# Kernel tuning notes

Measured on AMD Instinct MI355X. Metric: run time of the kernel, lower is better.

The kernel has to match this reference:

```python
import jax, jax.numpy as jnp
import numpy as np

N_EMBED = 64
HEAD_SIZE = 64
B, T = 4096, 128

def setup_inputs() -> dict:
    key = jax.random.key(0)
    k0, k1, k2, k3 = jax.random.split(key, 4)
    x = jax.random.normal(k0, (B, T, N_EMBED), dtype=jnp.float32)
    # nn.Linear(N_EMBED, head_size, bias=False): weight shape [head_size, N_EMBED], y = x @ W.T
    Wq = jax.random.normal(k1, (HEAD_SIZE, N_EMBED), dtype=jnp.float32) * (1.0 / np.sqrt(N_EMBED))
    Wk = jax.random.normal(k2, (HEAD_SIZE, N_EMBED), dtype=jnp.float32) * (1.0 / np.sqrt(N_EMBED))
    Wv = jax.random.normal(k3, (HEAD_SIZE, N_EMBED), dtype=jnp.float32) * (1.0 / np.sqrt(N_EMBED))
    return {"x": x, "Wq": Wq, "Wk": Wk, "Wv": Wv}

def reference(x, Wq, Wk, Wv):
    # q,k,v: [B,T,H]
    q = jnp.einsum('btc,hc->bth', x, Wq)
    k = jnp.einsum('btc,hc->bth', x, Wk)
    v = jnp.einsum('btc,hc->bth', x, Wv)
    scale = HEAD_SIZE ** -0.5
    scores = jnp.einsum('bth,bsh->bts', q, k) * scale  # [B,T,T]
    Tdim = x.shape[1]
    causal = jnp.tril(jnp.ones((Tdim, Tdim), dtype=bool))
    scores = jnp.where(causal, scores, -jnp.inf)
    weights = jax.nn.softmax(scores, axis=-1)
    # dropout disabled (eval mode) for deterministic reference
    out = jnp.einsum('bts,bsh->bth', weights, v)  # [B,T,H]
    return out
```

## Files before the change

kernel.cpp:

```cpp
#include <hip/hip_runtime.h>

#define KS 76
#define VS 140

typedef float f4  __attribute__((ext_vector_type(4)));
typedef short s8v __attribute__((ext_vector_type(8)));
typedef short s4v __attribute__((ext_vector_type(4)));

#define MFMA16(a, b, c) __builtin_amdgcn_mfma_f32_16x16x32_bf16((a), (b), (c), 0, 0, 0)

__device__ __forceinline__ unsigned short f2bf(float f) {
  union { float f; unsigned u; } x; x.f = f;
  unsigned r = x.u + 0x7FFFu + ((x.u >> 16) & 1u);
  return (unsigned short)(r >> 16);
}
__device__ __forceinline__ float bf2f(unsigned short s) {
  union { unsigned u; float f; } x; x.u = ((unsigned)s) << 16; return x.f;
}
__device__ __forceinline__ s8v cvt8(const float* p) {
  float4 a = *(const float4*)p;
  float4 b = *(const float4*)(p + 4);
  s8v v;
  v[0] = (short)f2bf(a.x); v[1] = (short)f2bf(a.y);
  v[2] = (short)f2bf(a.z); v[3] = (short)f2bf(a.w);
  v[4] = (short)f2bf(b.x); v[5] = (short)f2bf(b.y);
  v[6] = (short)f2bf(b.z); v[7] = (short)f2bf(b.w);
  return v;
}
__device__ __forceinline__ unsigned pack2(float a, float b) {
  return (unsigned)f2bf(a) | ((unsigned)f2bf(b) << 16);
}
__device__ __forceinline__ s8v mk8(unsigned a0, unsigned a1, unsigned b0, unsigned b1) {
  union { unsigned u[4]; s8v v; } r;
  r.u[0] = a0; r.u[1] = a1; r.u[2] = b0; r.u[3] = b1;
  return r.v;
}
__device__ __forceinline__ s8v ld44(const short* p0, const short* p1) {
  s4v a = *(const s4v*)p0;
  s4v b = *(const s4v*)(p1);
  s8v r;
  r[0] = a[0]; r[1] = a[1]; r[2] = a[2]; r[3] = a[3];
  r[4] = b[0]; r[5] = b[1]; r[6] = b[2]; r[7] = b[3];
  return r;
}

__global__ __launch_bounds__(256, 3)
void attn_head(const void* __restrict__ xg, const void* __restrict__ wqg,
               const void* __restrict__ wkg, const void* __restrict__ wvg,
               void* __restrict__ outg) {
  __shared__ __align__(16) short smem[18688];
  short* Ksm = smem;
  short* Vt  = smem + 9728;

  const int tid  = threadIdx.x;
  const int wave = tid >> 6;
  const int lane = tid & 63;
  const int c16  = lane & 15;
  const int quad = lane >> 4;
  const int b    = blockIdx.x;

  int ok;
  {
    const unsigned short* w = (const unsigned short*)wqg;
    float f = bf2f(w[tid]);
    float a = fabsf(f);
    ok = (f == 0.0f || (a >= 1e-4f && a <= 1e4f)) ? 1 : 0;
  }
  const int isbf = (__syncthreads_count(ok) >= 230) ? 1 : 0;

  const int mts[2] = {wave, 7 - wave};

  s8v xf[2][2];
  #pragma unroll
  for (int mi = 0; mi < 2; mi++) {
    const size_t base = (size_t)b * (128 * 64) + (size_t)(mts[mi] * 16 + c16) * 64;
    #pragma unroll
    for (int kt = 0; kt < 2; kt++) {
      const int off = kt * 32 + quad * 8;
      if (isbf) xf[mi][kt] = *(const s8v*)((const unsigned short*)xg + base + off);
      else      xf[mi][kt] = cvt8((const float*)xg + base + off);
    }
  }

  f4 QT[2][4];
  #pragma unroll
  for (int ht = 0; ht < 4; ht++) {
    s8v wqf[2], wkf[2], wvf[2];
    const int woff0 = (ht * 16 + c16) * 64 + quad * 8;
    #pragma unroll
    for (int kt = 0; kt < 2; kt++) {
      const int off = woff0 + kt * 32;
      if (isbf) {
        wqf[kt] = *(const s8v*)((const unsigned short*)wqg + off);
        wkf[kt] = *(const s8v*)((const unsigned short*)wkg + off);
        wvf[kt] = *(const s8v*)((const unsigned short*)wvg + off);
      } else {
        wqf[kt] = cvt8((const float*)wqg + off);
        wkf[kt] = cvt8((const float*)wkg + off);
        wvf[kt] = cvt8((const float*)wvg + off);
      }
    }
    #pragma unroll
    for (int mi = 0; mi < 2; mi++) {
      const int m = mts[mi];
      f4 z = {0.f, 0.f, 0.f, 0.f};
      f4 qt = z, kk = z, vv = z;
      qt = MFMA16(wqf[0], xf[mi][0], qt);  qt = MFMA16(wqf[1], xf[mi][1], qt);
      kk = MFMA16(xf[mi][0], wkf[0], kk);  kk = MFMA16(xf[mi][1], wkf[1], kk);
      vv = MFMA16(xf[mi][0], wvf[0], vv);  vv = MFMA16(xf[mi][1], wvf[1], vv);
      QT[mi][ht] = qt;
      #pragma unroll
      for (int r = 0; r < 4; r++)
        Ksm[(m * 16 + quad * 4 + r) * KS + ht * 16 + c16] = (short)f2bf(kk[r]);
      s4v pv;
      pv[0] = (short)f2bf(vv[0]); pv[1] = (short)f2bf(vv[1]);
      pv[2] = (short)f2bf(vv[2]); pv[3] = (short)f2bf(vv[3]);
      *(s4v*)(Vt + (ht * 16 + c16) * VS + m * 16 + quad * 4) = pv;
    }
  }

  s8v qb[2][2];
  #pragma unroll
  for (int mi = 0; mi < 2; mi++)
    #pragma unroll
    for (int hp = 0; hp < 2; hp++)
      qb[mi][hp] = mk8(
          pack2(QT[mi][2*hp][0]   * 0.125f, QT[mi][2*hp][1]   * 0.125f),
          pack2(QT[mi][2*hp][2]   * 0.125f, QT[mi][2*hp][3]   * 0.125f),
          pack2(QT[mi][2*hp+1][0] * 0.125f, QT[mi][2*hp+1][1] * 0.125f),
          pack2(QT[mi][2*hp+1][2] * 0.125f, QT[mi][2*hp+1][3] * 0.125f));

  __syncthreads();

  #pragma unroll
  for (int mi = 0; mi < 2; mi++) {
    const int m = mts[mi];

    f4 S[8];
    #pragma unroll
    for (int nt = 0; nt < 8; nt++) {
      if (nt > m) continue;
      const short* kr = Ksm + (nt * 16 + c16) * KS + quad * 4;
      f4 s = {0.f, 0.f, 0.f, 0.f};
      s = MFMA16(ld44(kr,      kr + 16), qb[mi][0], s);
      s = MFMA16(ld44(kr + 32, kr + 48), qb[mi][1], s);
      S[nt] = s;
    }

    float sum = 0.f;
    #pragma unroll
    for (int nt = 0; nt < 8; nt++) {
      if (nt > m) continue;
      #pragma unroll
      for (int r = 0; r < 4; r++) {
        const bool keep = (nt < m) || (quad * 4 + r <= c16);
        float e = keep ? __expf(S[nt][r]) : 0.0f;
        S[nt][r] = e;
        sum += e;
      }
    }
    sum += __shfl_xor(sum, 16);
    sum += __shfl_xor(sum, 32);
    const float inv = 1.0f / sum;

    unsigned ppk[8][2];
    #pragma unroll
    for (int nt = 0; nt < 8; nt++) {
      if (nt > m) continue;
      ppk[nt][0] = pack2(S[nt][0], S[nt][1]);
      ppk[nt][1] = pack2(S[nt][2], S[nt][3]);
    }

    f4 acc[4];
    #pragma unroll
    for (int ht = 0; ht < 4; ht++) { f4 z = {0.f,0.f,0.f,0.f}; acc[ht] = z; }
    const int nchunk = (m >> 1) + 1;
    #pragma unroll
    for (int kt = 0; kt < 4; kt++) {
      if (kt >= nchunk) continue;
      const bool hb = (2 * kt + 1) <= m;
      const s8v pb = mk8(ppk[2 * kt][0], ppk[2 * kt][1],
                         hb ? ppk[2 * kt + 1][0] : 0u,
                         hb ? ppk[2 * kt + 1][1] : 0u);
      #pragma unroll
      for (int ht = 0; ht < 4; ht++) {
        const short* vr = Vt + (ht * 16 + c16) * VS + kt * 32 + quad * 4;
        acc[ht] = MFMA16(ld44(vr, vr + 16), pb, acc[ht]);
      }
    }

    if (isbf) {
      unsigned short* op = (unsigned short*)outg + (size_t)b * (128 * 64);
      #pragma unroll
      for (int ht = 0; ht < 4; ht++) {
        s4v o;
        o[0] = (short)f2bf(acc[ht][0] * inv); o[1] = (short)f2bf(acc[ht][1] * inv);
        o[2] = (short)f2bf(acc[ht][2] * inv); o[3] = (short)f2bf(acc[ht][3] * inv);
        *(s4v*)(op + (size_t)(m * 16 + c16) * 64 + ht * 16 + quad * 4) = o;
      }
    } else {
      float* op = (float*)outg + (size_t)b * (128 * 64);
      #pragma unroll
      for (int ht = 0; ht < 4; ht++) {
        float4 o = {acc[ht][0] * inv, acc[ht][1] * inv,
                    acc[ht][2] * inv, acc[ht][3] * inv};
        *(float4*)(op + (size_t)(m * 16 + c16) * 64 + ht * 16 + quad * 4) = o;
      }
    }
  }
}

extern "C" void kernel_launch(void* const* d_in, const int* in_sizes, int n_in,
                              void* d_out, int out_size, void* d_ws, size_t ws_size,
                              hipStream_t stream) {
  (void)d_ws; (void)ws_size; (void)in_sizes; (void)n_in; (void)out_size;
  attn_head<<<dim3(4096), dim3(256), 0, stream>>>(
      d_in[0], d_in[1], d_in[2], d_in[3], d_out);
}
```

Before: 316.2 us.

## Swizzle K/V LDS layout, use packed bf16 converts, raise occupancy

Replaces the padded K and V^T shared-memory tiles (strides 76/140) with unpadded 64/128-wide tiles using an XOR swizzle keyed on the row. K is now computed transposed so each lane writes a packed 4-element vector instead of four scalar stores. Manual bf16 rounding is replaced by the packed float2-to-bfloat162 conversion intrinsic. The dtype-detection check becomes a per-wave ballot, which removes a block barrier. LDS shrinks to 32KB and launch bounds go from 3 to 5 blocks per SIMD to allow more resident blocks, at the risk of extra register pressure or spills.

```diff
diff --git a/kernel.cpp b/kernel.cpp
--- a/kernel.cpp
+++ b/kernel.cpp
@@ -1,7 +1,5 @@
 #include <hip/hip_runtime.h>
-
-#define KS 76
-#define VS 140
+#include <hip/hip_bf16.h>
 
 typedef float f4  __attribute__((ext_vector_type(4)));
 typedef short s8v __attribute__((ext_vector_type(8)));
@@ -9,10 +7,11 @@
 
 #define MFMA16(a, b, c) __builtin_amdgcn_mfma_f32_16x16x32_bf16((a), (b), (c), 0, 0, 0)
 
-__device__ __forceinline__ unsigned short f2bf(float f) {
-  union { float f; unsigned u; } x; x.f = f;
-  unsigned r = x.u + 0x7FFFu + ((x.u >> 16) & 1u);
-  return (unsigned short)(r >> 16);
+__device__ __forceinline__ unsigned cvtpk(float a, float b) {
+  __hip_bfloat162 h2 = __float22bfloat162_rn(make_float2(a, b));
+  unsigned u;
+  __builtin_memcpy(&u, &h2, 4);
+  return u;
 }
 __device__ __forceinline__ float bf2f(unsigned short s) {
   union { unsigned u; float f; } x; x.u = ((unsigned)s) << 16; return x.f;
@@ -20,15 +19,10 @@
 __device__ __forceinline__ s8v cvt8(const float* p) {
   float4 a = *(const float4*)p;
   float4 b = *(const float4*)(p + 4);
-  s8v v;
-  v[0] = (short)f2bf(a.x); v[1] = (short)f2bf(a.y);
-  v[2] = (short)f2bf(a.z); v[3] = (short)f2bf(a.w);
-  v[4] = (short)f2bf(b.x); v[5] = (short)f2bf(b.y);
-  v[6] = (short)f2bf(b.z); v[7] = (short)f2bf(b.w);
-  return v;
-}
-__device__ __forceinline__ unsigned pack2(float a, float b) {
-  return (unsigned)f2bf(a) | ((unsigned)f2bf(b) << 16);
+  union { unsigned u[4]; s8v v; } r;
+  r.u[0] = cvtpk(a.x, a.y); r.u[1] = cvtpk(a.z, a.w);
+  r.u[2] = cvtpk(b.x, b.y); r.u[3] = cvtpk(b.z, b.w);
+  return r.v;
 }
 __device__ __forceinline__ s8v mk8(unsigned a0, unsigned a1, unsigned b0, unsigned b1) {
   union { unsigned u[4]; s8v v; } r;
@@ -37,20 +31,20 @@
 }
 __device__ __forceinline__ s8v ld44(const short* p0, const short* p1) {
   s4v a = *(const s4v*)p0;
-  s4v b = *(const s4v*)(p1);
+  s4v b = *(const s4v*)p1;
   s8v r;
   r[0] = a[0]; r[1] = a[1]; r[2] = a[2]; r[3] = a[3];
   r[4] = b[0]; r[5] = b[1]; r[6] = b[2]; r[7] = b[3];
   return r;
 }
 
-__global__ __launch_bounds__(256, 3)
+__global__ __launch_bounds__(256, 5)
 void attn_head(const void* __restrict__ xg, const void* __restrict__ wqg,
                const void* __restrict__ wkg, const void* __restrict__ wvg,
                void* __restrict__ outg) {
-  __shared__ __align__(16) short smem[18688];
+  __shared__ __align__(16) short smem[16384];
   short* Ksm = smem;
-  short* Vt  = smem + 9728;
+  short* Vt  = smem + 8192;
 
   const int tid  = threadIdx.x;
   const int wave = tid >> 6;
@@ -58,15 +52,17 @@
   const int c16  = lane & 15;
   const int quad = lane >> 4;
   const int b    = blockIdx.x;
-
-  int ok;
+  const int swz  = c16 << 2;
+
+  int isbf;
   {
     const unsigned short* w = (const unsigned short*)wqg;
-    float f = bf2f(w[tid]);
+    float f = bf2f(w[lane]);
     float a = fabsf(f);
-    ok = (f == 0.0f || (a >= 1e-4f && a <= 1e4f)) ? 1 : 0;
-  }
-  const int isbf = (__syncthreads_count(ok) >= 230) ? 1 : 0;
+    int ok = (f == 0.0f || (a >= 1e-4f && a <= 1e4f)) ? 1 : 0;
+    unsigned long long ball = __ballot(ok);
+    isbf = (__popcll(ball) >= 58) ? 1 : 0;
+  }
 
   const int mts[2] = {wave, 7 - wave};
 
@@ -106,16 +102,19 @@
       f4 z = {0.f, 0.f, 0.f, 0.f};
       f4 qt = z, kk = z, vv = z;
       qt = MFMA16(wqf[0], xf[mi][0], qt);  qt = MFMA16(wqf[1], xf[mi][1], qt);
-      kk = MFMA16(xf[mi][0], wkf[0], kk);  kk = MFMA16(xf[mi][1], wkf[1], kk);
+      kk = MFMA16(wkf[0], xf[mi][0], kk);  kk = MFMA16(wkf[1], xf[mi][1], kk);
       vv = MFMA16(xf[mi][0], wvf[0], vv);  vv = MFMA16(xf[mi][1], wvf[1], vv);
       QT[mi][ht] = qt;
-      #pragma unroll
-      for (int r = 0; r < 4; r++)
-        Ksm[(m * 16 + quad * 4 + r) * KS + ht * 16 + c16] = (short)f2bf(kk[r]);
-      s4v pv;
-      pv[0] = (short)f2bf(vv[0]); pv[1] = (short)f2bf(vv[1]);
-      pv[2] = (short)f2bf(vv[2]); pv[3] = (short)f2bf(vv[3]);
-      *(s4v*)(Vt + (ht * 16 + c16) * VS + m * 16 + quad * 4) = pv;
+      {
+        union { unsigned u[2]; s4v v; } pk;
+        pk.u[0] = cvtpk(kk[0], kk[1]); pk.u[1] = cvtpk(kk[2], kk[3]);
+        *(s4v*)(Ksm + (m * 16 + c16) * 64 + ((ht * 16 + quad * 4) ^ swz)) = pk.v;
+      }
+      {
+        union { unsigned u[2]; s4v v; } pv;
+        pv.u[0] = cvtpk(vv[0], vv[1]); pv.u[1] = cvtpk(vv[2], vv[3]);
+        *(s4v*)(Vt + (ht * 16 + c16) * 128 + ((m * 16 + quad * 4) ^ swz)) = pv.v;
+      }
     }
   }
 
@@ -125,25 +124,26 @@
     #pragma unroll
     for (int hp = 0; hp < 2; hp++)
       qb[mi][hp] = mk8(
-          pack2(QT[mi][2*hp][0]   * 0.125f, QT[mi][2*hp][1]   * 0.125f),
-          pack2(QT[mi][2*hp][2]   * 0.125f, QT[mi][2*hp][3]   * 0.125f),
-          pack2(QT[mi][2*hp+1][0] * 0.125f, QT[mi][2*hp+1][1] * 0.125f),
-          pack2(QT[mi][2*hp+1][2] * 0.125f, QT[mi][2*hp+1][3] * 0.125f));
+          cvtpk(QT[mi][2*hp][0]   * 0.125f, QT[mi][2*hp][1]   * 0.125f),
+          cvtpk(QT[mi][2*hp][2]   * 0.125f, QT[mi][2*hp][3]   * 0.125f),
+          cvtpk(QT[mi][2*hp+1][0] * 0.125f, QT[mi][2*hp+1][1] * 0.125f),
+          cvtpk(QT[mi][2*hp+1][2] * 0.125f, QT[mi][2*hp+1][3] * 0.125f));
 
   __syncthreads();
 
   #pragma unroll
   for (int mi = 0; mi < 2; mi++) {
     const int m = mts[mi];
+    const int q4 = quad * 4;
 
     f4 S[8];
     #pragma unroll
     for (int nt = 0; nt < 8; nt++) {
       if (nt > m) continue;
-      const short* kr = Ksm + (nt * 16 + c16) * KS + quad * 4;
+      const short* kr = Ksm + (nt * 16 + c16) * 64;
       f4 s = {0.f, 0.f, 0.f, 0.f};
-      s = MFMA16(ld44(kr,      kr + 16), qb[mi][0], s);
-      s = MFMA16(ld44(kr + 32, kr + 48), qb[mi][1], s);
+      s = MFMA16(ld44(kr + ((q4     ) ^ swz), kr + ((q4 + 16) ^ swz)), qb[mi][0], s);
+      s = MFMA16(ld44(kr + ((q4 + 32) ^ swz), kr + ((q4 + 48) ^ swz)), qb[mi][1], s);
       S[nt] = s;
     }
 
@@ -153,7 +153,7 @@
       if (nt > m) continue;
       #pragma unroll
       for (int r = 0; r < 4; r++) {
-        const bool keep = (nt < m) || (quad * 4 + r <= c16);
+        const bool keep = (nt < m) || (q4 + r <= c16);
         float e = keep ? __expf(S[nt][r]) : 0.0f;
         S[nt][r] = e;
         sum += e;
@@ -167,8 +167,8 @@
     #pragma unroll
     for (int nt = 0; nt < 8; nt++) {
       if (nt > m) continue;
-      ppk[nt][0] = pack2(S[nt][0], S[nt][1]);
-      ppk[nt][1] = pack2(S[nt][2], S[nt][3]);
+      ppk[nt][0] = cvtpk(S[nt][0], S[nt][1]);
+      ppk[nt][1] = cvtpk(S[nt][2], S[nt][3]);
     }
 
     f4 acc[4];
@@ -184,8 +184,10 @@
                          hb ? ppk[2 * kt + 1][1] : 0u);
       #pragma unroll
       for (int ht = 0; ht < 4; ht++) {
-        const short* vr = Vt + (ht * 16 + c16) * VS + kt * 32 + quad * 4;
-        acc[ht] = MFMA16(ld44(vr, vr + 16), pb, acc[ht]);
+        const short* vr = Vt + (ht * 16 + c16) * 128;
+        const s8v va = ld44(vr + ((kt * 32 + q4     ) ^ swz),
+                            vr + ((kt * 32 + q4 + 16) ^ swz));
+        acc[ht] = MFMA16(va, pb, acc[ht]);
       }
     }
 
@@ -193,10 +195,10 @@
       unsigned short* op = (unsigned short*)outg + (size_t)b * (128 * 64);
       #pragma unroll
       for (int ht = 0; ht < 4; ht++) {
-        s4v o;
-        o[0] = (short)f2bf(acc[ht][0] * inv); o[1] = (short)f2bf(acc[ht][1] * inv);
-        o[2] = (short)f2bf(acc[ht][2] * inv); o[3] = (short)f2bf(acc[ht][3] * inv);
-        *(s4v*)(op + (size_t)(m * 16 + c16) * 64 + ht * 16 + quad * 4) = o;
+        union { unsigned u[2]; s4v v; } o;
+        o.u[0] = cvtpk(acc[ht][0] * inv, acc[ht][1] * inv);
+        o.u[1] = cvtpk(acc[ht][2] * inv, acc[ht][3] * inv);
+        *(s4v*)(op + (size_t)(m * 16 + c16) * 64 + ht * 16 + q4) = o.v;
       }
     } else {
       float* op = (float*)outg + (size_t)b * (128 * 64);
@@ -204,7 +206,7 @@
       for (int ht = 0; ht < 4; ht++) {
         float4 o = {acc[ht][0] * inv, acc[ht][1] * inv,
                     acc[ht][2] * inv, acc[ht][3] * inv};
-        *(float4*)(op + (size_t)(m * 16 + c16) * 64 + ht * 16 + quad * 4) = o;
+        *(float4*)(op + (size_t)(m * 16 + c16) * 64 + ht * 16 + q4) = o;
       }
     }
   }
```

Result: slower. 356.2 us (+12.7%).
